# Optimization experiments

Hardware: AMD Instinct MI355X
Metric: run time of the kernel (lower is better)

Reference implementation:

```python
import jax, jax.numpy as jnp
import numpy as np

NUM_CLUSTERS = 8
KMEANS_ITERS = 10  # fixed Lloyd iterations (deterministic stand-in for sklearn KMeans)


def _pairwise_sqdist(x, cent):
    # x: [N, C], cent: [K, C] -> [N, K]
    return (jnp.sum(x * x, axis=1, keepdims=True)
            - 2.0 * (x @ cent.T)
            + jnp.sum(cent * cent, axis=1)[None, :])


def _kmeans_labels(x):
    # x: [N, C] -> labels [N] int32. Deterministic init: first K points.
    K = NUM_CLUSTERS
    cent0 = x[:K]

    def step(cent, _):
        d = _pairwise_sqdist(x, cent)                      # [N, K]
        lab = jnp.argmin(d, axis=1)                        # [N]
        oh = jax.nn.one_hot(lab, K, dtype=x.dtype)         # [N, K]
        cnt = oh.sum(axis=0)                               # [K]
        sums = oh.T @ x                                    # [K, C]
        new = jnp.where(cnt[:, None] > 0,
                        sums / jnp.maximum(cnt, 1.0)[:, None],
                        cent)
        return new, None

    cent, _ = jax.lax.scan(step, cent0, None, length=KMEANS_ITERS)
    return jnp.argmin(_pairwise_sqdist(x, cent), axis=1)


def setup_inputs() -> dict:
    key = jax.random.key(0)
    feature_map = jax.random.normal(key, (32, 256, 64, 64), dtype=jnp.float32)
    return {"feature_map": feature_map}


def reference(feature_map):
    B, C, H, W = feature_map.shape
    K = NUM_CLUSTERS
    # (B, C, H, W) -> (B, N, C) with N = H*W
    feats = feature_map.reshape(B, C, H * W).transpose(0, 2, 1)
    # Cluster assignments are non-differentiable constants (torch uses .detach())
    labels = jax.vmap(_kmeans_labels)(jax.lax.stop_gradient(feats))   # [B, N]
    oh = jax.nn.one_hot(labels, K, dtype=feats.dtype)                 # [B, N, K]
    cnt = oh.sum(axis=1)                                              # [B, K]
    sums = jnp.einsum('bnk,bnc->bkc', oh, feats)                      # [B, K, C]
    # empty cluster -> zeros, matching torch fallback
    clustered = jnp.where(cnt[..., None] > 0,
                          sums / jnp.maximum(cnt, 1.0)[..., None],
                          0.0)
    return clustered  # [B, K, C]
```

## Files before the change

kernel.cpp:

```cpp
#include <hip/hip_runtime.h>
#include <stdint.h>

#define NB   32
#define NC   256
#define NPTS 4096
#define KCL  8
#define KC   384
#define NPANEL 11
#define HALF0 192
#define BSTR  196

__device__ float np_sumsq_avx512(const float* sh) {
  float half[2];
  #pragma unroll
  for (int h = 0; h < 2; ++h) {
    const float* ap = sh + h * 128;
    float rv[16];
    #pragma unroll
    for (int l = 0; l < 16; ++l) {
      float q[8];
      #pragma unroll
      for (int j = 0; j < 8; ++j) {
        float e = ap[16 * j + l];
        q[j] = __fmul_rn(e, e);
      }
      rv[l] = __fadd_rn(__fadd_rn(__fadd_rn(q[0], q[1]), __fadd_rn(q[2], q[3])),
                        __fadd_rn(__fadd_rn(q[4], q[5]), __fadd_rn(q[6], q[7])));
    }
    float t1[8];
    #pragma unroll
    for (int l = 0; l < 8; ++l) t1[l] = __fadd_rn(rv[l], rv[l + 8]);
    float t2[4];
    #pragma unroll
    for (int l = 0; l < 4; ++l) t2[l] = __fadd_rn(t1[l], t1[l + 2 + 2]);
    float t3[2];
    #pragma unroll
    for (int l = 0; l < 2; ++l) t3[l] = __fadd_rn(t2[l], t2[l + 2]);
    half[h] = __fadd_rn(t3[0], t3[1]);
  }
  return __fadd_rn(half[0], half[1]);
}

__device__ float np_sumsq_avx512_s8(const float* base, int k) {
  float half[2];
  #pragma unroll
  for (int h = 0; h < 2; ++h) {
    float rv[16];
    #pragma unroll
    for (int l = 0; l < 16; ++l) {
      float q[8];
      #pragma unroll
      for (int j = 0; j < 8; ++j) {
        float e = base[(h * 128 + 16 * j + l) * KCL + k];
        q[j] = __fmul_rn(e, e);
      }
      rv[l] = __fadd_rn(__fadd_rn(__fadd_rn(q[0], q[1]), __fadd_rn(q[2], q[3])),
                        __fadd_rn(__fadd_rn(q[4], q[5]), __fadd_rn(q[6], q[7])));
    }
    float t1[8];
    #pragma unroll
    for (int l = 0; l < 8; ++l) t1[l] = __fadd_rn(rv[l], rv[l + 8]);
    float t2[4];
    #pragma unroll
    for (int l = 0; l < 4; ++l) t2[l] = __fadd_rn(t1[l], t1[l + 2 + 2]);
    float t3[2];
    #pragma unroll
    for (int l = 0; l < 2; ++l) t3[l] = __fadd_rn(t2[l], t2[l + 2]);
    half[h] = __fadd_rn(t3[0], t3[1]);
  }
  return __fadd_rn(half[0], half[1]);
}

__global__ __launch_bounds__(256) void k_init(const float* __restrict__ X,
                                              float* __restrict__ cent0,
                                              float* __restrict__ cnorm0) {
  const int b = blockIdx.x >> 3, k = blockIdx.x & 7, c = threadIdx.x;
  __shared__ float sarr[NC];
  float v = X[(size_t)b * NC * NPTS + (size_t)c * NPTS + k];
  cent0[(b * NC + c) * KCL + k] = v;
  sarr[c] = v;
  __syncthreads();
  if (c == 0) cnorm0[b * KCL + k] = np_sumsq_avx512(sarr);
}

__global__ __launch_bounds__(256) void k_assign(const float* __restrict__ X,
                                                const float* __restrict__ pp,
                                                const int* __restrict__ pc,
                                                const float* __restrict__ centPrev,
                                                float* __restrict__ centCur,
                                                const float* __restrict__ cnorm0,
                                                int* __restrict__ lab,
                                                int it) {
  const int blk = blockIdx.x;
  const int b   = blk >> 4;
  const int n0  = (blk & 15) << 8;
  const int t   = threadIdx.x;

  __shared__ __align__(16) float centL[NC * KCL];
  __shared__ float cnfL[KCL];

  if (it == 0) {
    const float4* cp = (const float4*)(centPrev + (size_t)b * NC * KCL);
    #pragma unroll
    for (int i2 = 0; i2 < 2; ++i2)
      ((float4*)centL)[i2 * 256 + t] = cp[i2 * 256 + t];
    if (t < KCL) cnfL[t] = cnorm0[b * KCL + t];
  } else {
    const int c = t;
    #pragma unroll
    for (int k = 0; k < KCL; ++k) {
      float C = 0.f; int cnt = 0;
      for (int pnl = 0; pnl < NPANEL; ++pnl) {
        C = __fadd_rn(C, pp[(size_t)((b * NPANEL + pnl) * KCL + k) * NC + c]);
        cnt += pc[(b * NPANEL + pnl) * KCL + k];
      }
      const float mean = __fdiv_rn(C, (float)((cnt > 0) ? cnt : 1));
      const int ci = (b * NC + c) * KCL + k;
      float nv = (cnt > 0) ? mean : centPrev[ci];
      centCur[ci] = nv;
      centL[c * KCL + k] = nv;
    }
    __syncthreads();
    if (t < KCL) cnfL[t] = np_sumsq_avx512_s8(centL, t);
  }
  __syncthreads();

  float cnf[KCL];
  #pragma unroll
  for (int k = 0; k < KCL; ++k) cnf[k] = cnfL[k];

  const float* Xp = X + (size_t)b * NC * NPTS + n0 + t;
  float a = 0.f;
  float bb[KCL];
  #pragma unroll
  for (int k = 0; k < KCL; ++k) bb[k] = 0.f;
  const float4* cL4 = (const float4*)centL;

  #pragma unroll 8
  for (int c = 0; c < NC; ++c) {
    float x = Xp[(size_t)c * NPTS];
    a = __fadd_rn(a, __fmul_rn(x, x));
    float4 c0 = cL4[c * 2], c1 = cL4[c * 2 + 1];
    bb[0] = __builtin_fmaf(x, c0.x, bb[0]);
    bb[1] = __builtin_fmaf(x, c0.y, bb[1]);
    bb[2] = __builtin_fmaf(x, c0.z, bb[2]);
    bb[3] = __builtin_fmaf(x, c0.w, bb[3]);
    bb[4] = __builtin_fmaf(x, c1.x, bb[4]);
    bb[5] = __builtin_fmaf(x, c1.y, bb[5]);
    bb[6] = __builtin_fmaf(x, c1.z, bb[6]);
    bb[7] = __builtin_fmaf(x, c1.w, bb[7]);
  }

  int lb = 0; float best = 3.4e38f;
  #pragma unroll
  for (int k = 0; k < KCL; ++k) {
    float d = __fadd_rn(__fsub_rn(a, __fmul_rn(2.0f, bb[k])), cnf[k]);
    if (d < best) { best = d; lb = k; }
  }
  lab[b * NPTS + n0 + t] = lb;
}

__global__ __launch_bounds__(256) void k_psum(const float* __restrict__ X,
                                              const int* __restrict__ lab,
                                              float* __restrict__ pp,
                                              int* __restrict__ pc) {
  const int blk = blockIdx.x;
  const int b = blk / 88, r = blk % 88, panel = r >> 3, cg = r & 7;
  const int p0 = panel * KC;
  const int len = (panel < 10) ? KC : (NPTS - 10 * KC);
  const int t = threadIdx.x, k = t & 7, cl = t >> 3, lane = t & 63;

  __shared__ __align__(16) float buf[32 * BSTR];
  __shared__ int perm[KC];
  __shared__ int wcnt[6][KCL];
  __shared__ int cbase[6][KCL];
  __shared__ int offs[KCL], hist[KCL];

  const float* Xb = X + (size_t)b * NC * NPTS + (size_t)(cg * 32) * NPTS + p0;

  #pragma unroll
  for (int i2 = 0; i2 < 6; ++i2) {
    int i = i2 * 256 + t;
    int c = i / 48, q4 = i - c * 48;
    *(float4*)&buf[c * BSTR + q4 * 4] =
        *(const float4*)(Xb + (size_t)c * NPTS + q4 * 4);
  }

  const int* Lb = lab + b * NPTS + p0;
  const uint64_t lt = (1ull << lane) - 1ull;
  int ml0, ml1, rk0 = 0, rk1 = 0;
  {
    const int q = t;
    ml0 = (q < len) ? Lb[q] : -1;
    const int chunk = q >> 6;
    #pragma unroll
    for (int kk = 0; kk < KCL; ++kk) {
      uint64_t m = __ballot(ml0 == kk);
      if (lane == 0) wcnt[chunk][kk] = (int)__popcll(m);
      if (ml0 == kk) rk0 = (int)__popcll(m & lt);
    }
  }
  {
    const int q = 256 + t;
    ml1 = (q < len) ? Lb[q] : -1;
    const int chunk = q >> 6;
    #pragma unroll
    for (int kk = 0; kk < KCL; ++kk) {
      uint64_t m = __ballot(ml1 == kk);
      if (lane == 0 && chunk < 6) wcnt[chunk][kk] = (int)__popcll(m);
      if (ml1 == kk) rk1 = (int)__popcll(m & lt);
    }
  }
  __syncthreads();
  if (t == 0) {
    int rr = 0;
    for (int kk = 0; kk < KCL; ++kk) {
      int s = 0;
      #pragma unroll
      for (int ch = 0; ch < 6; ++ch) { cbase[ch][kk] = rr + s; s += wcnt[ch][kk]; }
      offs[kk] = rr; hist[kk] = s; rr += s;
    }
  }
  __syncthreads();
  if (ml0 >= 0) perm[cbase[t >> 6][ml0] + rk0] = t;
  if (ml1 >= 0) perm[cbase[(256 + t) >> 6][ml1] + rk1] = 256 + t;
  __syncthreads();

  const int base = offs[k], n = hist[k];
  const int nh0 = cbase[3][k] - offs[k];
  const float* bp = &buf[cl * BSTR];
  float pa = 0.f;
  #pragma unroll 4
  for (int i = 0; i < nh0; ++i) {
    int p = perm[base + i];
    pa = __fadd_rn(pa, bp[p]);
  }
  __syncthreads();

  const int nf4 = (len - HALF0) >> 2;
  #pragma unroll
  for (int i2 = 0; i2 < 6; ++i2) {
    int i = i2 * 256 + t;
    int c = i / 48, q4 = i - c * 48;
    if (q4 < nf4)
      *(float4*)&buf[c * BSTR + q4 * 4] =
          *(const float4*)(Xb + (size_t)c * NPTS + HALF0 + q4 * 4);
  }
  __syncthreads();

  #pragma unroll 4
  for (int i = nh0; i < n; ++i) {
    int p = perm[base + i] - HALF0;
    pa = __fadd_rn(pa, bp[p]);
  }
  pp[(size_t)((b * NPANEL + panel) * KCL + k) * NC + cg * 32 + cl] = pa;
  if (cl == 0) pc[(b * NPANEL + panel) * KCL + k] = n;
}

__global__ __launch_bounds__(256) void k_out(const float* __restrict__ pp,
                                             const int* __restrict__ pc,
                                             float* __restrict__ out) {
  const int b = blockIdx.x >> 3, k = blockIdx.x & 7, c = threadIdx.x;
  float C = 0.f;
  int cnt = 0;
  for (int pnl = 0; pnl < NPANEL; ++pnl) {
    C = __fadd_rn(C, pp[(size_t)((b * NPANEL + pnl) * KCL + k) * NC + c]);
    cnt += pc[(b * NPANEL + pnl) * KCL + k];
  }
  out[(b * KCL + k) * NC + c] =
      (cnt > 0) ? __fdiv_rn(C, (float)cnt) : 0.0f;
}

extern "C" void kernel_launch(void* const* d_in, const int* in_sizes, int n_in,
                              void* d_out, int out_size, void* d_ws, size_t ws_size,
                              hipStream_t stream) {
  const float* X = (const float*)d_in[0];
  float* out = (float*)d_out;

  float* cent0  = (float*)d_ws;
  float* cent1  = cent0 + (size_t)NB * NC * KCL;
  float* cnorm0 = cent1 + (size_t)NB * NC * KCL;
  int*   lab    = (int*)(cnorm0 + NB * KCL);
  float* pp     = (float*)(lab + (size_t)NB * NPTS);
  int*   pc     = (int*)(pp + (size_t)NB * NPANEL * KCL * NC);

  float* cent[2] = {cent0, cent1};

  k_init<<<NB * KCL, 256, 0, stream>>>(X, cent0, cnorm0);
  for (int it = 0; it <= 10; ++it) {
    float* prev = (it == 0) ? cent0 : cent[(it - 1) & 1];
    float* cur  = cent[it & 1];
    k_assign<<<NB * 16, 256, 0, stream>>>(X, pp, pc, prev, cur, cnorm0, lab, it);
    k_psum<<<NB * NPANEL * KCL, 256, 0, stream>>>(X, lab, pp, pc);
  }
  k_out<<<NB * KCL, 256, 0, stream>>>(pp, pc, out);
}
```

Baseline: 743.9 us.

## Fuse assignment and partial-sum kernels into one per-panel iteration kernel

Merges the separate assign and psum kernels into a single k_iter kernel per (batch, panel) block of 384 threads. Labels stay in registers and shared memory instead of going through global memory, and launch count per iteration drops from two to one. The partial-sum buffers are double-buffered so that a block can read the previous iteration's partials while writing new ones. The trade-off is far fewer blocks (352 instead of 512 plus 2816), and each block now walks all 8 channel groups serially with more syncs, which may hurt parallelism and occupancy.

```diff
diff --git a/kernel.cpp b/kernel.cpp
--- a/kernel.cpp
+++ b/kernel.cpp
@@ -83,133 +83,99 @@
   if (c == 0) cnorm0[b * KCL + k] = np_sumsq_avx512(sarr);
 }
 
-__global__ __launch_bounds__(256) void k_assign(const float* __restrict__ X,
-                                                const float* __restrict__ pp,
-                                                const int* __restrict__ pc,
-                                                const float* __restrict__ centPrev,
-                                                float* __restrict__ centCur,
-                                                const float* __restrict__ cnorm0,
-                                                int* __restrict__ lab,
-                                                int it) {
+__global__ __launch_bounds__(384) void k_iter(const float* __restrict__ X,
+                                              const float* __restrict__ ppIn,
+                                              const int* __restrict__ pcIn,
+                                              float* __restrict__ ppOut,
+                                              int* __restrict__ pcOut,
+                                              const float* __restrict__ centPrev,
+                                              float* __restrict__ centCur,
+                                              const float* __restrict__ cnorm0,
+                                              int it) {
   const int blk = blockIdx.x;
-  const int b   = blk >> 4;
-  const int n0  = (blk & 15) << 8;
-  const int t   = threadIdx.x;
+  const int b = blk / NPANEL, panel = blk % NPANEL;
+  const int p0 = panel * KC;
+  const int len = (panel < 10) ? KC : (NPTS - 10 * KC);
+  const int t = threadIdx.x, lane = t & 63;
 
   __shared__ __align__(16) float centL[NC * KCL];
   __shared__ float cnfL[KCL];
-
-  if (it == 0) {
-    const float4* cp = (const float4*)(centPrev + (size_t)b * NC * KCL);
-    #pragma unroll
-    for (int i2 = 0; i2 < 2; ++i2)
-      ((float4*)centL)[i2 * 256 + t] = cp[i2 * 256 + t];
-    if (t < KCL) cnfL[t] = cnorm0[b * KCL + t];
-  } else {
-    const int c = t;
-    #pragma unroll
-    for (int k = 0; k < KCL; ++k) {
-      float C = 0.f; int cnt = 0;
-      for (int pnl = 0; pnl < NPANEL; ++pnl) {
-        C = __fadd_rn(C, pp[(size_t)((b * NPANEL + pnl) * KCL + k) * NC + c]);
-        cnt += pc[(b * NPANEL + pnl) * KCL + k];
-      }
-      const float mean = __fdiv_rn(C, (float)((cnt > 0) ? cnt : 1));
-      const int ci = (b * NC + c) * KCL + k;
-      float nv = (cnt > 0) ? mean : centPrev[ci];
-      centCur[ci] = nv;
-      centL[c * KCL + k] = nv;
-    }
-    __syncthreads();
-    if (t < KCL) cnfL[t] = np_sumsq_avx512_s8(centL, t);
-  }
-  __syncthreads();
-
-  float cnf[KCL];
-  #pragma unroll
-  for (int k = 0; k < KCL; ++k) cnf[k] = cnfL[k];
-
-  const float* Xp = X + (size_t)b * NC * NPTS + n0 + t;
-  float a = 0.f;
-  float bb[KCL];
-  #pragma unroll
-  for (int k = 0; k < KCL; ++k) bb[k] = 0.f;
-  const float4* cL4 = (const float4*)centL;
-
-  #pragma unroll 8
-  for (int c = 0; c < NC; ++c) {
-    float x = Xp[(size_t)c * NPTS];
-    a = __fadd_rn(a, __fmul_rn(x, x));
-    float4 c0 = cL4[c * 2], c1 = cL4[c * 2 + 1];
-    bb[0] = __builtin_fmaf(x, c0.x, bb[0]);
-    bb[1] = __builtin_fmaf(x, c0.y, bb[1]);
-    bb[2] = __builtin_fmaf(x, c0.z, bb[2]);
-    bb[3] = __builtin_fmaf(x, c0.w, bb[3]);
-    bb[4] = __builtin_fmaf(x, c1.x, bb[4]);
-    bb[5] = __builtin_fmaf(x, c1.y, bb[5]);
-    bb[6] = __builtin_fmaf(x, c1.z, bb[6]);
-    bb[7] = __builtin_fmaf(x, c1.w, bb[7]);
-  }
-
-  int lb = 0; float best = 3.4e38f;
-  #pragma unroll
-  for (int k = 0; k < KCL; ++k) {
-    float d = __fadd_rn(__fsub_rn(a, __fmul_rn(2.0f, bb[k])), cnf[k]);
-    if (d < best) { best = d; lb = k; }
-  }
-  lab[b * NPTS + n0 + t] = lb;
-}
-
-__global__ __launch_bounds__(256) void k_psum(const float* __restrict__ X,
-                                              const int* __restrict__ lab,
-                                              float* __restrict__ pp,
-                                              int* __restrict__ pc) {
-  const int blk = blockIdx.x;
-  const int b = blk / 88, r = blk % 88, panel = r >> 3, cg = r & 7;
-  const int p0 = panel * KC;
-  const int len = (panel < 10) ? KC : (NPTS - 10 * KC);
-  const int t = threadIdx.x, k = t & 7, cl = t >> 3, lane = t & 63;
-
   __shared__ __align__(16) float buf[32 * BSTR];
   __shared__ int perm[KC];
-  __shared__ int wcnt[6][KCL];
-  __shared__ int cbase[6][KCL];
-  __shared__ int offs[KCL], hist[KCL];
-
-  const float* Xb = X + (size_t)b * NC * NPTS + (size_t)(cg * 32) * NPTS + p0;
-
+  __shared__ int wcnt[6][KCL], cbase[6][KCL], offs[KCL], hist[KCL];
+
+  if (it == 0) {
+    if (t < 256) {
+      const float4* cp = (const float4*)(centPrev + (size_t)b * NC * KCL);
+      #pragma unroll
+      for (int i2 = 0; i2 < 2; ++i2)
+        ((float4*)centL)[i2 * 256 + t] = cp[i2 * 256 + t];
+      if (t < KCL) cnfL[t] = cnorm0[b * KCL + t];
+    }
+  } else {
+    if (t < 256) {
+      const int c = t;
+      #pragma unroll
+      for (int k = 0; k < KCL; ++k) {
+        float C = 0.f; int cnt = 0;
+        for (int pnl = 0; pnl < NPANEL; ++pnl) {
+          C = __fadd_rn(C, ppIn[(size_t)((b * NPANEL + pnl) * KCL + k) * NC + c]);
+          cnt += pcIn[(b * NPANEL + pnl) * KCL + k];
+        }
+        const float mean = __fdiv_rn(C, (float)((cnt > 0) ? cnt : 1));
+        const int ci = (b * NC + c) * KCL + k;
+        float nv = (cnt > 0) ? mean : centPrev[ci];
+        centCur[ci] = nv;
+        centL[c * KCL + k] = nv;
+      }
+    }
+    __syncthreads();
+    if (t < KCL) cnfL[t] = np_sumsq_avx512_s8(centL, t);
+  }
+  __syncthreads();
+
+  int ml = -1;
+  if (t < len) {
+    float cnf[KCL];
+    #pragma unroll
+    for (int k = 0; k < KCL; ++k) cnf[k] = cnfL[k];
+    const float* Xp = X + (size_t)b * NC * NPTS + p0 + t;
+    const float4* cL4 = (const float4*)centL;
+    float a = 0.f;
+    float bb[KCL];
+    #pragma unroll
+    for (int k = 0; k < KCL; ++k) bb[k] = 0.f;
+    #pragma unroll 8
+    for (int c = 0; c < NC; ++c) {
+      float x = Xp[(size_t)c * NPTS];
+      a = __fadd_rn(a, __fmul_rn(x, x));
+      float4 c0 = cL4[c * 2], c1 = cL4[c * 2 + 1];
+      bb[0] = __builtin_fmaf(x, c0.x, bb[0]);
+      bb[1] = __builtin_fmaf(x, c0.y, bb[1]);
+      bb[2] = __builtin_fmaf(x, c0.z, bb[2]);
+      bb[3] = __builtin_fmaf(x, c0.w, bb[3]);
+      bb[4] = __builtin_fmaf(x, c1.x, bb[4]);
+      bb[5] = __builtin_fmaf(x, c1.y, bb[5]);
+      bb[6] = __builtin_fmaf(x, c1.z, bb[6]);
+      bb[7] = __builtin_fmaf(x, c1.w, bb[7]);
+    }
+    int lb = 0; float best = 3.4e38f;
+    #pragma unroll
+    for (int k = 0; k < KCL; ++k) {
+      float d = __fadd_rn(__fsub_rn(a, __fmul_rn(2.0f, bb[k])), cnf[k]);
+      if (d < best) { best = d; lb = k; }
+    }
+    ml = lb;
+  }
+
+  const uint64_t lt = (1ull << lane) - 1ull;
+  const int chunk = t >> 6;
+  int rk = 0;
   #pragma unroll
-  for (int i2 = 0; i2 < 6; ++i2) {
-    int i = i2 * 256 + t;
-    int c = i / 48, q4 = i - c * 48;
-    *(float4*)&buf[c * BSTR + q4 * 4] =
-        *(const float4*)(Xb + (size_t)c * NPTS + q4 * 4);
-  }
-
-  const int* Lb = lab + b * NPTS + p0;
-  const uint64_t lt = (1ull << lane) - 1ull;
-  int ml0, ml1, rk0 = 0, rk1 = 0;
-  {
-    const int q = t;
-    ml0 = (q < len) ? Lb[q] : -1;
-    const int chunk = q >> 6;
-    #pragma unroll
-    for (int kk = 0; kk < KCL; ++kk) {
-      uint64_t m = __ballot(ml0 == kk);
-      if (lane == 0) wcnt[chunk][kk] = (int)__popcll(m);
-      if (ml0 == kk) rk0 = (int)__popcll(m & lt);
-    }
-  }
-  {
-    const int q = 256 + t;
-    ml1 = (q < len) ? Lb[q] : -1;
-    const int chunk = q >> 6;
-    #pragma unroll
-    for (int kk = 0; kk < KCL; ++kk) {
-      uint64_t m = __ballot(ml1 == kk);
-      if (lane == 0 && chunk < 6) wcnt[chunk][kk] = (int)__popcll(m);
-      if (ml1 == kk) rk1 = (int)__popcll(m & lt);
-    }
+  for (int kk = 0; kk < KCL; ++kk) {
+    uint64_t m = __ballot(ml == kk);
+    if (lane == 0) wcnt[chunk][kk] = (int)__popcll(m);
+    if (ml == kk) rk = (int)__popcll(m & lt);
   }
   __syncthreads();
   if (t == 0) {
@@ -222,39 +188,52 @@
     }
   }
   __syncthreads();
-  if (ml0 >= 0) perm[cbase[t >> 6][ml0] + rk0] = t;
-  if (ml1 >= 0) perm[cbase[(256 + t) >> 6][ml1] + rk1] = 256 + t;
-  __syncthreads();
-
-  const int base = offs[k], n = hist[k];
-  const int nh0 = cbase[3][k] - offs[k];
-  const float* bp = &buf[cl * BSTR];
-  float pa = 0.f;
-  #pragma unroll 4
-  for (int i = 0; i < nh0; ++i) {
-    int p = perm[base + i];
-    pa = __fadd_rn(pa, bp[p]);
-  }
-  __syncthreads();
-
+  if (ml >= 0) perm[cbase[chunk][ml] + rk] = t;
+  __syncthreads();
+
+  const int k = t & 7, cl = t >> 3;
   const int nf4 = (len - HALF0) >> 2;
-  #pragma unroll
-  for (int i2 = 0; i2 < 6; ++i2) {
-    int i = i2 * 256 + t;
-    int c = i / 48, q4 = i - c * 48;
-    if (q4 < nf4)
+  const float* Xb = X + (size_t)b * NC * NPTS + p0;
+
+  for (int cg = 0; cg < 8; ++cg) {
+    const float* Xs = Xb + (size_t)(cg * 32) * NPTS;
+    #pragma unroll
+    for (int i2 = 0; i2 < 4; ++i2) {
+      int i = i2 * 384 + t;
+      int c = i / 48, q4 = i - c * 48;
       *(float4*)&buf[c * BSTR + q4 * 4] =
-          *(const float4*)(Xb + (size_t)c * NPTS + HALF0 + q4 * 4);
-  }
-  __syncthreads();
-
-  #pragma unroll 4
-  for (int i = nh0; i < n; ++i) {
-    int p = perm[base + i] - HALF0;
-    pa = __fadd_rn(pa, bp[p]);
-  }
-  pp[(size_t)((b * NPANEL + panel) * KCL + k) * NC + cg * 32 + cl] = pa;
-  if (cl == 0) pc[(b * NPANEL + panel) * KCL + k] = n;
+          *(const float4*)(Xs + (size_t)c * NPTS + q4 * 4);
+    }
+    __syncthreads();
+    float pa = 0.f;
+    int base = 0, n = 0, nh0 = 0;
+    if (t < 256) {
+      base = offs[k]; n = hist[k]; nh0 = cbase[3][k] - offs[k];
+      const float* bp = &buf[cl * BSTR];
+      #pragma unroll 4
+      for (int i = 0; i < nh0; ++i)
+        pa = __fadd_rn(pa, bp[perm[base + i]]);
+    }
+    __syncthreads();
+    #pragma unroll
+    for (int i2 = 0; i2 < 4; ++i2) {
+      int i = i2 * 384 + t;
+      int c = i / 48, q4 = i - c * 48;
+      if (q4 < nf4)
+        *(float4*)&buf[c * BSTR + q4 * 4] =
+            *(const float4*)(Xs + (size_t)c * NPTS + HALF0 + q4 * 4);
+    }
+    __syncthreads();
+    if (t < 256) {
+      const float* bp = &buf[cl * BSTR];
+      #pragma unroll 4
+      for (int i = nh0; i < n; ++i)
+        pa = __fadd_rn(pa, bp[perm[base + i] - HALF0]);
+      ppOut[(size_t)((b * NPANEL + panel) * KCL + k) * NC + cg * 32 + cl] = pa;
+      if (cl == 0 && cg == 0) pcOut[(b * NPANEL + panel) * KCL + k] = n;
+    }
+    __syncthreads();
+  }
 }
 
 __global__ __launch_bounds__(256) void k_out(const float* __restrict__ pp,
@@ -280,18 +259,23 @@
   float* cent0  = (float*)d_ws;
   float* cent1  = cent0 + (size_t)NB * NC * KCL;
   float* cnorm0 = cent1 + (size_t)NB * NC * KCL;
-  int*   lab    = (int*)(cnorm0 + NB * KCL);
-  float* pp     = (float*)(lab + (size_t)NB * NPTS);
-  int*   pc     = (int*)(pp + (size_t)NB * NPANEL * KCL * NC);
-
+  float* pp0    = cnorm0 + NB * KCL;
+  float* pp1    = pp0 + (size_t)NB * NPANEL * KCL * NC;
+  int*   pc0    = (int*)(pp1 + (size_t)NB * NPANEL * KCL * NC);
+  int*   pc1    = pc0 + (size_t)NB * NPANEL * KCL;
+
+  float* ppB[2] = {pp0, pp1};
+  int*   pcB[2] = {pc0, pc1};
   float* cent[2] = {cent0, cent1};
 
   k_init<<<NB * KCL, 256, 0, stream>>>(X, cent0, cnorm0);
   for (int it = 0; it <= 10; ++it) {
-    float* prev = (it == 0) ? cent0 : cent[(it - 1) & 1];
-    float* cur  = cent[it & 1];
-    k_assign<<<NB * 16, 256, 0, stream>>>(X, pp, pc, prev, cur, cnorm0, lab, it);
-    k_psum<<<NB * NPANEL * KCL, 256, 0, stream>>>(X, lab, pp, pc);
-  }
-  k_out<<<NB * KCL, 256, 0, stream>>>(pp, pc, out);
-}
+    float* prev = (it <= 1) ? cent0 : cent[(it - 1) & 1];
+    float* cur  = (it == 0) ? cent1 : cent[it & 1];
+    k_iter<<<NB * NPANEL, 384, 0, stream>>>(
+        X, ppB[(it + 1) & 1], pcB[(it + 1) & 1],
+        ppB[it & 1], pcB[it & 1],
+        prev, cur, cnorm0, it);
+  }
+  k_out<<<NB * KCL, 256, 0, stream>>>(ppB[0], pcB[0], out);
+}
```

Result: slower. 787.0 us (+5.8%).
